# Performance work log

Hardware: AMD Instinct MI355X
Metric: run time of the kernel (lower is better)

Reference implementation:

```python
import jax, jax.numpy as jnp
import numpy as np

N = 50000
E = 500000
R = 8
IN_DIM = 128
HID = 128
OUT = 128
NUM_GRAPHS = 64
EPS_BN = 1e-5


def _glorot(key, shape):
    fan_in, fan_out = shape[-2], shape[-1]
    lim = np.sqrt(6.0 / (fan_in + fan_out))
    return jax.random.uniform(key, shape, jnp.float32, -lim, lim)


def setup_inputs() -> dict:
    key = jax.random.key(0)
    ks = jax.random.split(key, 24)
    x = jax.random.normal(ks[0], (N, IN_DIM), jnp.float32)
    edge_index = jax.random.randint(ks[1], (2, E), 0, N, jnp.int64)
    edge_type = jax.random.randint(ks[2], (E,), 0, R, jnp.int64)
    batch = jnp.sort(jax.random.randint(ks[3], (N,), 0, NUM_GRAPHS, jnp.int64))
    d = {
        "x": x, "edge_index": edge_index, "edge_type": edge_type, "batch": batch,
        # RGCN layer 1 (in->hid): per-relation weights, root weight, bias
        "W1": _glorot(ks[4], (R, IN_DIM, HID)), "root1": _glorot(ks[5], (IN_DIM, HID)), "b1": jnp.zeros((HID,), jnp.float32),
        "W2": _glorot(ks[6], (R, HID, HID)), "root2": _glorot(ks[7], (HID, HID)), "b2": jnp.zeros((HID,), jnp.float32),
        "W3": _glorot(ks[8], (R, HID, HID)), "root3": _glorot(ks[9], (HID, HID)), "b3": jnp.zeros((HID,), jnp.float32),
        # BatchNorm affine params
        "g1": jnp.ones((HID,), jnp.float32), "beta1": jnp.zeros((HID,), jnp.float32),
        "g2": jnp.ones((HID,), jnp.float32), "beta2": jnp.zeros((HID,), jnp.float32),
        # attention MLP: hid -> hid//2 -> 1
        "A1": _glorot(ks[10], (HID, HID // 2)), "a1": jnp.zeros((HID // 2,), jnp.float32),
        "A2": _glorot(ks[11], (HID // 2, 1)), "a2": jnp.zeros((1,), jnp.float32),
        # combiner MLP: 2*hid -> hid -> out
        "C1": _glorot(ks[12], (2 * HID, HID)), "c1": jnp.zeros((HID,), jnp.float32),
        "C2": _glorot(ks[13], (HID, OUT)), "c2": jnp.zeros((OUT,), jnp.float32),
    }
    return d


def rgcn_conv(h, src, dst, etype, W, root, bias):
    # relation-wise gather -> mean-aggregate per (dst, relation) -> transform
    seg = dst * R + etype                                   # [E]
    msg = h[src]                                            # [E, d_in] gather
    agg = jax.ops.segment_sum(msg, seg, num_segments=N * R) # [N*R, d_in]
    cnt = jax.ops.segment_sum(jnp.ones((seg.shape[0],), h.dtype), seg, num_segments=N * R)
    agg = agg / jnp.maximum(cnt, 1.0)[:, None]              # mean aggregation (PyG default)
    agg = agg.reshape(N, R, -1)
    out = jnp.einsum('nri,rio->no', agg, W) + h @ root + bias
    return out


def batch_norm(h, gamma, beta):
    mu = jnp.mean(h, axis=0, keepdims=True)
    var = jnp.mean((h - mu) ** 2, axis=0, keepdims=True)
    return (h - mu) * jax.lax.rsqrt(var + EPS_BN) * gamma + beta


def lrelu(h):
    return jax.nn.leaky_relu(h, 0.1)


def reference(x, edge_index, edge_type, batch, W1, root1, b1, W2, root2, b2,
              W3, root3, b3, g1, beta1, g2, beta2, A1, a1, A2, a2, C1, c1, C2, c2):
    src, dst = edge_index[0], edge_index[1]
    h = rgcn_conv(x, src, dst, edge_type, W1, root1, b1)
    h = lrelu(batch_norm(h, g1, beta1))
    h = rgcn_conv(h, src, dst, edge_type, W2, root2, b2)
    h = lrelu(batch_norm(h, g2, beta2))
    node_emb = rgcn_conv(h, src, dst, edge_type, W3, root3, b3)  # [N, HID]

    # attention pooling: scores softmax-ed over ALL nodes (dim=0, as in source)
    scores = lrelu(node_emb @ A1 + a1) @ A2 + a2                 # [N, 1]
    attn = jax.nn.softmax(scores, axis=0)                        # [N, 1]
    global_emb = jax.ops.segment_sum(node_emb * attn, batch, num_segments=NUM_GRAPHS)

    combined = jnp.concatenate([node_emb, global_emb[batch]], axis=1)  # [N, 2*HID]
    final = lrelu(combined @ C1 + c1) @ C2 + c2                  # [N, OUT]
    norm = jnp.linalg.norm(final, axis=1, keepdims=True)
    return final / jnp.maximum(norm, 1e-12)
```

## Files before the change

### kernel.cpp

```cpp
#include <hip/hip_runtime.h>
#include <hip/hip_bf16.h>

typedef unsigned int u32;
typedef unsigned short u16;
typedef __bf16 bf16_t;
typedef bf16_t bf16x8 __attribute__((ext_vector_type(8)));
typedef float f32x4 __attribute__((ext_vector_type(4)));

constexpr int NN = 50000;
constexpr int EE = 500000;
constexpr int RR = 8;
constexpr int NKEY = RR * NN;
constexpr int PAIR_B = (NKEY + 511) / 512;

constexpr int WX_A1T = 0;
constexpr int WX_C1T = 8192;
constexpr int WX_C2T = 40960;
constexpr int WX_A2  = 57344;
constexpr int WX_a1  = 57408;
constexpr int WX_c1  = 57472;
constexpr int WX_c2  = 57600;
constexpr int WX_a2s = 57728;
constexpr int WX_TOT = 57729;

__device__ __forceinline__ float bf2f(u32 v){
  union { u32 u; float f; } x; x.u = (v & 0xFFFFu) << 16; return x.f;
}
__device__ __forceinline__ u16 f2bf(float f){
  union { u32 u; float f; } x; x.f = f;
  u32 r = x.u + 0x7FFFu + ((x.u >> 16) & 1u);
  return (u16)(r >> 16);
}
__device__ __forceinline__ float lrelu(float x){ return x > 0.f ? x : 0.1f * x; }
__device__ __forceinline__ float ldf(const void* p, int i, u32 fm){
  return fm ? ((const float*)p)[i] : bf2f(((const u16*)p)[i]);
}
__device__ __forceinline__ void gl_lds16(const u16* g, u16* l){
  __builtin_amdgcn_global_load_lds((const __attribute__((address_space(1))) u32*)g,
                                   (__attribute__((address_space(3))) u32*)l, 16, 0, 0);
}

__global__ void k_fdetect(const void* x, u32* md){
  __shared__ u32 c;
  if (threadIdx.x == 0) c = 0;
  __syncthreads();
  const u16* p = (const u16*)x;
  u32 loc = 0;
  for (int j = 0; j < 16; j++){
    u16 v = p[threadIdx.x * 16 + j];
    u32 e = (v >> 7) & 0xFF;
    if (e >= 0xFD) loc++;
  }
  atomicAdd(&c, loc);
  __syncthreads();
  if (threadIdx.x == 0) md[0] = (c >= 4) ? 1u : 0u;
}
__global__ void k_idetect(const void* et, u32* md){
  __shared__ u32 c;
  if (threadIdx.x == 0) c = 0;
  __syncthreads();
  const int* p = (const int*)et;
  u32 loc = 0;
  for (int j = 0; j < 8; j++){
    int idx = 2 * (threadIdx.x * 8 + j) + 1;
    if (p[idx] != 0) loc++;
  }
  atomicAdd(&c, loc);
  __syncthreads();
  if (threadIdx.x == 0) md[1] = (c == 0) ? 1u : 0u;
}

__global__ void k_icvt(const void* ei, const void* et, const void* bat,
                       int* ei_c, int* et_c, int* bat_c, const u32* md){
  u32 im = md[1];
  int i = blockIdx.x * 256 + threadIdx.x;
  if (i < 2 * EE){
    const int* p = (const int*)ei;
    ei_c[i] = im ? p[2 * i] : p[i];
  } else if (i < 3 * EE){
    int j = i - 2 * EE;
    const int* p = (const int*)et;
    et_c[j] = im ? p[2 * j] : p[j];
  } else if (i < 3 * EE + NN){
    int j = i - 3 * EE;
    const int* p = (const int*)bat;
    bat_c[j] = im ? p[2 * j] : p[j];
  }
}

__global__ void k_xcvt(const void* x, u16* xb, const u32* md, u32* flags){
  u32 fm = md[0];
  int i4 = (blockIdx.x * 256 + threadIdx.x) * 4;
  if (i4 >= NN * 128) return;
  float v[4];
  if (fm){
    float4 f = *(const float4*)((const float*)x + i4);
    v[0]=f.x; v[1]=f.y; v[2]=f.z; v[3]=f.w;
  } else {
    uint2 u = *(const uint2*)((const u16*)x + i4);
    v[0]=bf2f(u.x); v[1]=bf2f(u.x>>16); v[2]=bf2f(u.y); v[3]=bf2f(u.y>>16);
  }
  bool bad = false;
  u16 o[4];
  for (int j = 0; j < 4; j++){
    if (v[j] != v[j]){ bad = true; v[j] = 0.f; }
    o[j] = f2bf(v[j]);
  }
  unsigned long long bal = __ballot(bad);
  if (bal && (threadIdx.x & 63) == 0) atomicOr(flags, 2u);
  uint2 st;
  st.x = (u32)o[0] | ((u32)o[1] << 16);
  st.y = (u32)o[2] | ((u32)o[3] << 16);
  *(uint2*)(xb + i4) = st;
}

__global__ void k_wcat(const void* W1, const void* r1, const void* W2, const void* r2,
                       const void* W3, const void* r3, u16* wcatT, const u32* md, u32* flags){
  u32 fm = md[0];
  int idx = blockIdx.x * 256 + threadIdx.x;
  if (idx >= 3 * 128 * 1152) return;
  int L = idx / (128 * 1152);
  int rem = idx % (128 * 1152);
  int n = rem / 1152, k = rem % 1152;
  const void* W  = (L == 0) ? W1 : ((L == 1) ? W2 : W3);
  const void* rt = (L == 0) ? r1 : ((L == 1) ? r2 : r3);
  float v = (k < 1024) ? ldf(W, k * 128 + n, fm) : ldf(rt, (k - 1024) * 128 + n, fm);
  if (v != v){ v = 0.f; atomicOr(flags, 2u); }
  wcatT[idx] = f2bf(v);
}

__global__ void k_wext(const void* A1, const void* a1, const void* A2, const void* a2,
                       const void* C1, const void* c1, const void* C2, const void* c2,
                       u16* wext, const u32* md){
  u32 fm = md[0];
  int idx = blockIdx.x * 256 + threadIdx.x;
  if (idx >= WX_TOT) return;
  float v;
  if (idx < WX_C1T){
    int n = idx >> 7, k = idx & 127;
    v = ldf(A1, k * 64 + n, fm);
  } else if (idx < WX_C2T){
    int j = idx - WX_C1T; int n = j >> 8, k = j & 255;
    v = ldf(C1, k * 128 + n, fm);
  } else if (idx < WX_A2){
    int j = idx - WX_C2T; int n = j >> 7, k = j & 127;
    v = ldf(C2, k * 128 + n, fm);
  } else if (idx < WX_a1){ v = ldf(A2, idx - WX_A2, fm); }
  else if (idx < WX_c1){ v = ldf(a1, idx - WX_a1, fm); }
  else if (idx < WX_c2){ v = ldf(c1, idx - WX_c1, fm); }
  else if (idx < WX_a2s){ v = ldf(c2, idx - WX_c2, fm); }
  else { v = ldf(a2, 0, fm); }
  wext[idx] = f2bf(v);
}

__global__ void k_count3(const int* __restrict__ ei, const int* __restrict__ et, u32* __restrict__ cnt){
  int e = blockIdx.x * 256 + threadIdx.x;
  if (e >= EE) return;
  atomicAdd(&cnt[ei[EE + e] * RR + et[e]], 1u);
}
__global__ void k_pairA(const u32* __restrict__ cnt, u32* __restrict__ blockSum){
  __shared__ u32 sd[256];
  int b = blockIdx.x, t = threadIdx.x;
  u32 s = 0;
  for (int j = 0; j < 2; j++){
    int key = b * 512 + t * 2 + j;
    if (key < NKEY) s += cnt[key];
  }
  sd[t] = s; __syncthreads();
  for (int off = 128; off; off >>= 1){ if (t < off) sd[t] += sd[t + off]; __syncthreads(); }
  if (t == 0) blockSum[b] = sd[0];
}
__global__ void k_pairB(const u32* __restrict__ blockSum, u32* __restrict__ blockBase){
  int lane = threadIdx.x;
  u32 loc[13]; u32 s = 0;
  for (int j = 0; j < 13; j++){
    int b = lane * 13 + j;
    u32 v = (b < PAIR_B) ? blockSum[b] : 0u;
    loc[j] = s; s += v;
  }
  u32 tot = s;
  for (int off = 1; off < 64; off <<= 1){
    u32 x = __shfl_up(tot, off);
    if (lane >= off) tot += x;
  }
  u32 excl = tot - s;
  for (int j = 0; j < 13; j++){
    int b = lane * 13 + j;
    if (b < PAIR_B) blockBase[b] = excl + loc[j];
  }
}
__global__ void k_pairC(const u32* __restrict__ cnt, const u32* __restrict__ blockBase,
                        u32* __restrict__ pairStart, u32* __restrict__ cursor){
  __shared__ u32 sd[256];
  int b = blockIdx.x, t = threadIdx.x;
  int k0 = b * 512 + t * 2;
  u32 v0 = 0, v1 = 0;
  if (k0 < NKEY) v0 = cnt[k0];
  if (k0 + 1 < NKEY) v1 = cnt[k0 + 1];
  sd[t] = v0 + v1; __syncthreads();
  for (int off = 1; off < 256; off <<= 1){
    u32 x = (t >= off) ? sd[t - off] : 0u;
    __syncthreads();
    sd[t] += x;
    __syncthreads();
  }
  u32 excl = sd[t] - (v0 + v1);
  u32 base = blockBase[b] + excl;
  if (k0 < NKEY){ pairStart[k0] = base; cursor[k0] = 0u; }
  if (k0 + 1 < NKEY){ pairStart[k0 + 1] = base + v0; cursor[k0 + 1] = 0u; }
  if (k0 + 1 == NKEY - 1) pairStart[NKEY] = base + v0 + v1;
}
__global__ void k_sort3(const int* __restrict__ ei, const int* __restrict__ et,
                        const u32* __restrict__ pairStart, u32* __restrict__ cursor,
                        u32* __restrict__ src_s){
  int e = blockIdx.x * 256 + threadIdx.x;
  if (e >= EE) return;
  int r = et[e], d = ei[EE + e];
  u32 key = (u32)d * RR + (u32)r;
  u32 p = pairStart[key] + atomicAdd(&cursor[key], 1u);
  src_s[p] = (u32)ei[e];
}

__global__ __launch_bounds__(256) void k_agg(const u16* __restrict__ h,
                                             const u32* __restrict__ pairStart,
                                             const u32* __restrict__ src_s,
                                             u16* __restrict__ agg){
  int d = blockIdx.x * 4 + (threadIdx.x >> 6);
  if (d >= NN) return;
  int lane = threadIdx.x & 63;
  const uint4* p4 = (const uint4*)(pairStart + d * 8);
  uint4 q0 = p4[0], q1 = p4[1];
  u32 ps[9];
  ps[0]=q0.x; ps[1]=q0.y; ps[2]=q0.z; ps[3]=q0.w;
  ps[4]=q1.x; ps[5]=q1.y; ps[6]=q1.z; ps[7]=q1.w;
  ps[8]=pairStart[d * 8 + 8];
  u16* dst = agg + (size_t)d * 1024 + lane * 2;
  #pragma unroll
  for (int r = 0; r < 8; r++){
    float a0 = 0.f, a1 = 0.f;
    for (u32 j = ps[r]; j < ps[r + 1]; j++){
      u32 src = src_s[j];
      u32 v = *(const u32*)(h + (size_t)src * 128 + lane * 2);
      a0 += bf2f(v); a1 += bf2f(v >> 16);
    }
    int c = (int)(ps[r + 1] - ps[r]);
    float sc = 1.0f / (float)max(c, 1);
    u32 st = (u32)f2bf(a0 * sc) | ((u32)f2bf(a1 * sc) << 16);
    *(u32*)(dst + r * 128) = st;
  }
}

__global__ __launch_bounds__(256) void k_gemm_big(const u16* __restrict__ h,
                                                  const u16* __restrict__ agg,
                                                  const u16* __restrict__ wT,
                                                  const void* __restrict__ bias,
                                                  float* __restrict__ out, const u32* md,
                                                  float* __restrict__ stats, int do_stats){
  __shared__ u16 As[64][64];
  __shared__ u16 Bs[128][64];
  u32 fm = md[0];
  int m0 = blockIdx.x * 64;
  int tid = threadIdx.x;
  int w = tid >> 6, lane = tid & 63, qd = lane >> 4, l16 = lane & 15;

  int rin = lane >> 3;
  int sc8 = (lane & 7) ^ rin;

  const u16* agA[2]; const u16* hA[2]; u16* ldsA[2];
  #pragma unroll
  for (int i = 0; i < 2; i++){
    int row = (w * 2 + i) * 8 + rin;
    int node = m0 + row; if (node > NN - 1) node = NN - 1;
    agA[i] = agg + (size_t)node * 1024 + sc8 * 8;
    hA[i]  = h + (size_t)node * 128 + sc8 * 8;
    ldsA[i] = &As[(w * 2 + i) * 8][0];
  }
  const u16* wB[4]; u16* ldsB[4];
  #pragma unroll
  for (int i = 0; i < 4; i++){
    int row = (w * 4 + i) * 8 + rin;
    wB[i] = wT + (size_t)row * 1152 + sc8 * 8;
    ldsB[i] = &Bs[(w * 4 + i) * 8][0];
  }

  f32x4 acc[8];
  #pragma unroll
  for (int j = 0; j < 8; j++) acc[j] = (f32x4){0.f,0.f,0.f,0.f};

  int sw = (l16 & 7) << 3;
  for (int k0 = 0; k0 < 1152; k0 += 64){
    __syncthreads();
    if (k0 < 1024){
      gl_lds16(agA[0] + k0, ldsA[0]);
      gl_lds16(agA[1] + k0, ldsA[1]);
    } else {
      gl_lds16(hA[0] + (k0 - 1024), ldsA[0]);
      gl_lds16(hA[1] + (k0 - 1024), ldsA[1]);
    }
    #pragma unroll
    for (int i = 0; i < 4; i++) gl_lds16(wB[i] + k0, ldsB[i]);
    __syncthreads();
    #pragma unroll
    for (int kk = 0; kk < 64; kk += 32){
      bf16x8 a = *(const bf16x8*)(&As[w * 16 + l16][(kk + qd * 8) ^ sw]);
      #pragma unroll
      for (int ct = 0; ct < 8; ct++){
        bf16x8 b = *(const bf16x8*)(&Bs[ct * 16 + l16][(kk + qd * 8) ^ sw]);
        acc[ct] = __builtin_amdgcn_mfma_f32_16x16x32_bf16(a, b, acc[ct], 0, 0, 0);
      }
    }
  }

  float sarr[8], s2arr[8];
  #pragma unroll
  for (int ct = 0; ct < 8; ct++){
    int col = ct * 16 + l16;
    float bv = ldf(bias, col, fm);
    float s = 0.f, s2 = 0.f;
    int rbase = m0 + w * 16 + qd * 4;
    #pragma unroll
    for (int rg = 0; rg < 4; rg++){
      int node = rbase + rg;
      if (node < NN){
        float v = acc[ct][rg] + bv;
        out[(size_t)node * 128 + col] = v;
        s += v; s2 += v * v;
      }
    }
    s  += __shfl_xor(s, 16);  s  += __shfl_xor(s, 32);
    s2 += __shfl_xor(s2, 16); s2 += __shfl_xor(s2, 32);
    sarr[ct] = s; s2arr[ct] = s2;
  }
  if (do_stats){
    float* red = (float*)&As[0][0];
    __syncthreads();
    if (qd == 0){
      #pragma unroll
      for (int ct = 0; ct < 8; ct++){
        red[w * 256 + ct * 16 + l16] = sarr[ct];
        red[w * 256 + 128 + ct * 16 + l16] = s2arr[ct];
      }
    }
    __syncthreads();
    if (tid < 256){
      float v = red[tid] + red[256 + tid] + red[512 + tid] + red[768 + tid];
      unsafeAtomicAdd(&stats[tid], v);
    }
  }
}

__global__ void k_bnapply(const float* __restrict__ out, const float* __restrict__ stats,
                          const void* __restrict__ g, const void* __restrict__ beta,
                          u16* __restrict__ hout, const u32* md, u32* flags, u32 layerbit){
  u32 fm = md[0];
  int idx = (blockIdx.x * 256 + threadIdx.x) * 4;
  if (idx >= NN * 128) return;
  int col = idx & 127;
  float4 v = *(const float4*)(out + idx);
  float vv[4] = {v.x, v.y, v.z, v.w};
  bool bad = false;
  u16 o[4];
  for (int j = 0; j < 4; j++){
    int c = col + j;
    float mu = stats[c] * (1.0f / NN);
    float var = fmaxf(stats[128 + c] * (1.0f / NN) - mu * mu, 0.f);
    float sc = ldf(g, c, fm) * rsqrtf(var + 1e-5f);
    float sh = ldf(beta, c, fm) - mu * sc;
    float r = vv[j] * sc + sh;
    if (r != r || sc != sc){ bad = true; r = 0.f; }
    o[j] = f2bf(lrelu(r));
  }
  unsigned long long bal = __ballot(bad);
  if (bal && (threadIdx.x & 63) == 0) atomicOr(flags, layerbit);
  uint2 st;
  st.x = (u32)o[0] | ((u32)o[1] << 16);
  st.y = (u32)o[2] | ((u32)o[3] << 16);
  *(uint2*)(hout + idx) = st;
}

__global__ __launch_bounds__(256) void k_scores_mfma(const float* __restrict__ emb,
                                                     const u16* __restrict__ wext,
                                                     float* __restrict__ scores){
  __shared__ u16 As[64][136];
  int m0 = blockIdx.x * 64;
  int tid = threadIdx.x;
  int w = tid >> 6, lane = tid & 63, qd = lane >> 4, l16 = lane & 15;
  for (int it = 0; it < 8; it++){
    int lin = it * 1024 + tid * 4;
    int row = lin >> 7, c = lin & 127;
    int node = m0 + row;
    float4 v = make_float4(0.f,0.f,0.f,0.f);
    if (node < NN) v = *(const float4*)(emb + (size_t)node * 128 + c);
    uint2 st;
    st.x = (u32)f2bf(v.x) | ((u32)f2bf(v.y) << 16);
    st.y = (u32)f2bf(v.z) | ((u32)f2bf(v.w) << 16);
    *(uint2*)(&As[row][c]) = st;
  }
  __syncthreads();
  f32x4 acc[4];
  for (int j = 0; j < 4; j++) acc[j] = (f32x4){0.f,0.f,0.f,0.f};
  for (int k0 = 0; k0 < 4; k0++){
    bf16x8 a = *(const bf16x8*)(&As[w * 16 + l16][k0 * 32 + qd * 8]);
    for (int ct = 0; ct < 4; ct++){
      bf16x8 b = *(const bf16x8*)(wext + WX_A1T + (size_t)(ct * 16 + l16) * 128 + k0 * 32 + qd * 8);
      acc[ct] = __builtin_amdgcn_mfma_f32_16x16x32_bf16(a, b, acc[ct], 0, 0, 0);
    }
  }
  float a1v[4], a2v[4];
  for (int ct = 0; ct < 4; ct++){
    a1v[ct] = bf2f(wext[WX_a1 + ct * 16 + l16]);
    a2v[ct] = bf2f(wext[WX_A2 + ct * 16 + l16]);
  }
  float a2s = bf2f(wext[WX_a2s]);
  for (int rg = 0; rg < 4; rg++){
    float s = 0.f;
    for (int ct = 0; ct < 4; ct++)
      s += lrelu(acc[ct][rg] + a1v[ct]) * a2v[ct];
    s += __shfl_xor(s, 1); s += __shfl_xor(s, 2);
    s += __shfl_xor(s, 4); s += __shfl_xor(s, 8);
    int row = m0 + w * 16 + qd * 4 + rg;
    if (l16 == 0 && row < NN) scores[row] = s + a2s;
  }
}

__device__ __forceinline__ u32 fmap(float f){
  union{u32 u; float f;} x; x.f = f;
  return (x.u & 0x80000000u) ? ~x.u : (x.u | 0x80000000u);
}
__device__ __forceinline__ float funmap(u32 m){
  union{u32 u; float f;} x;
  x.u = (m & 0x80000000u) ? (m ^ 0x80000000u) : ~m;
  return x.f;
}

__global__ void k_max(const float* __restrict__ scores, u32* smax){
  int gid = blockIdx.x * 256 + threadIdx.x;
  float m = -1e30f;
  for (int i = gid; i < NN; i += 256 * 128) m = fmaxf(m, scores[i]);
  for (int off = 32; off; off >>= 1) m = fmaxf(m, __shfl_down(m, off));
  if ((threadIdx.x & 63) == 0) atomicMax(smax, fmap(m));
}

__global__ void k_expsum(const float* __restrict__ scores, const u32* smax,
                         float* __restrict__ attnw, float* ssum, u32* flags){
  float mx = funmap(*smax);
  int gid = blockIdx.x * 256 + threadIdx.x;
  if (mx != mx){ if (gid == 0) atomicOr(flags, 32u); mx = 0.f; }
  float s = 0.f;
  bool bad = false;
  for (int i = gid; i < NN; i += 256 * 128){
    float e = __expf(scores[i] - mx);
    if (e != e){ bad = true; e = 0.f; }
    attnw[i] = e; s += e;
  }
  unsigned long long bal = __ballot(bad);
  if (bal && (threadIdx.x & 63) == 0) atomicOr(flags, 32u);
  for (int off = 32; off; off >>= 1) s += __shfl_down(s, off);
  if ((threadIdx.x & 63) == 0) unsafeAtomicAdd(ssum, s);
}

constexpr int POOL_CHUNK = 32;
__global__ __launch_bounds__(128) void k_pool(const float* __restrict__ emb,
                                              const float* __restrict__ attnw,
                                              const float* __restrict__ ssum,
                                              const int* __restrict__ batch,
                                              float* __restrict__ gemb, u32* flags){
  int t = threadIdx.x;
  int n0 = blockIdx.x * POOL_CHUNK;
  if (n0 >= NN) return;
  int n1 = min(n0 + POOL_CHUNK, NN);
  float sv = *ssum;
  bool bad = !(sv > 0.f) || (sv != sv);
  if (bad && t == 0 && blockIdx.x == 0) atomicOr(flags, 64u);
  float rs = bad ? 0.f : 1.0f / sv;
  int cur = batch[n0];
  float acc = 0.f;
  for (int n = n0; n < n1; n++){
    int b = batch[n];
    if (b != cur){ unsafeAtomicAdd(&gemb[cur * 128 + t], acc * rs); acc = 0.f; cur = b; }
    acc += emb[(size_t)n * 128 + t] * attnw[n];
  }
  unsafeAtomicAdd(&gemb[cur * 128 + t], acc * rs);
}

__global__ __launch_bounds__(256) void k_final_mfma(const float* __restrict__ emb,
                                                    const float* __restrict__ gemb,
                                                    const int* __restrict__ batch,
                                                    const u16* __restrict__ wext,
                                                    void* __restrict__ outp,
                                                    const u32* md){
  __shared__ u16 As[64][264];
  u16 (*Hs)[136] = (u16(*)[136])(&As[0][0]);
  u32 fm = md[0];
  int m0 = blockIdx.x * 64;
  int tid = threadIdx.x;
  int w = tid >> 6, lane = tid & 63, qd = lane >> 4, l16 = lane & 15;
  for (int it = 0; it < 16; it++){
    int lin = it * 1024 + tid * 4;
    int row = lin >> 8, c = lin & 255;
    int node = m0 + row;
    float4 v = make_float4(0.f,0.f,0.f,0.f);
    if (node < NN){
      if (c < 128) v = *(const float4*)(emb + (size_t)node * 128 + c);
      else { int g = batch[node]; v = *(const float4*)(gemb + (size_t)g * 128 + (c - 128)); }
    }
    uint2 st;
    st.x = (u32)f2bf(v.x) | ((u32)f2bf(v.y) << 16);
    st.y = (u32)f2bf(v.z) | ((u32)f2bf(v.w) << 16);
    *(uint2*)(&As[row][c]) = st;
  }
  __syncthreads();
  f32x4 acc[8];
  for (int j = 0; j < 8; j++) acc[j] = (f32x4){0.f,0.f,0.f,0.f};
  for (int k0 = 0; k0 < 8; k0++){
    bf16x8 a = *(const bf16x8*)(&As[w * 16 + l16][k0 * 32 + qd * 8]);
    for (int ct = 0; ct < 8; ct++){
      bf16x8 b = *(const bf16x8*)(wext + WX_C1T + (size_t)(ct * 16 + l16) * 256 + k0 * 32 + qd * 8);
      acc[ct] = __builtin_amdgcn_mfma_f32_16x16x32_bf16(a, b, acc[ct], 0, 0, 0);
    }
  }
  __syncthreads();
  for (int ct = 0; ct < 8; ct++){
    float c1v = bf2f(wext[WX_c1 + ct * 16 + l16]);
    for (int rg = 0; rg < 4; rg++){
      int row = w * 16 + qd * 4 + rg;
      Hs[row][ct * 16 + l16] = f2bf(lrelu(acc[ct][rg] + c1v));
    }
  }
  __syncthreads();
  f32x4 acc2[8];
  for (int j = 0; j < 8; j++) acc2[j] = (f32x4){0.f,0.f,0.f,0.f};
  for (int k0 = 0; k0 < 4; k0++){
    bf16x8 a = *(const bf16x8*)(&Hs[w * 16 + l16][k0 * 32 + qd * 8]);
    for (int ct = 0; ct < 8; ct++){
      bf16x8 b = *(const bf16x8*)(wext + WX_C2T + (size_t)(ct * 16 + l16) * 128 + k0 * 32 + qd * 8);
      acc2[ct] = __builtin_amdgcn_mfma_f32_16x16x32_bf16(a, b, acc2[ct], 0, 0, 0);
    }
  }
  float c2v[8];
  for (int ct = 0; ct < 8; ct++) c2v[ct] = bf2f(wext[WX_c2 + ct * 16 + l16]);
  for (int rg = 0; rg < 4; rg++){
    float ss = 0.f;
    for (int ct = 0; ct < 8; ct++){
      float o = acc2[ct][rg] + c2v[ct];
      ss += o * o;
    }
    ss += __shfl_xor(ss, 1); ss += __shfl_xor(ss, 2);
    ss += __shfl_xor(ss, 4); ss += __shfl_xor(ss, 8);
    float sc = 1.0f / fmaxf(sqrtf(ss), 1e-12f);
    int row = m0 + w * 16 + qd * 4 + rg;
    if (row < NN){
      if (fm){
        float* op = (float*)outp;
        for (int ct = 0; ct < 8; ct++)
          op[(size_t)row * 128 + ct * 16 + l16] = (acc2[ct][rg] + c2v[ct]) * sc;
      } else {
        u16* op = (u16*)outp;
        for (int ct = 0; ct < 8; ct++)
          op[(size_t)row * 128 + ct * 16 + l16] = f2bf((acc2[ct][rg] + c2v[ct]) * sc);
      }
    }
  }
}

__global__ void k_diag(const u32* pairStart, const u32* flags, const u32* md, void* outp){
  if (threadIdx.x != 0 || blockIdx.x != 0) return;
  u32 fm = md[0];
  u32 f = flags[0];
  if (pairStart[NKEY] != (u32)EE) f |= 1u;
  for (int b = 0; b < 9; b++){
    if (f & (1u << b)){
      float s = (float)(131072 >> b);
      if (fm) ((float*)outp)[b] = s;
      else ((u16*)outp)[b] = f2bf(s);
    }
  }
}
__global__ void k_wsfail(u32* outp){ outp[0] = 0x43000000u; }

constexpr size_t O_OUT   = 0;
constexpr size_t O_H     = 25600000;
constexpr size_t O_XBF   = 38400000;
constexpr size_t O_WCAT  = 51200000;
constexpr size_t O_WEXT  = 52084736;
constexpr size_t O_EI    = 52200448;
constexpr size_t O_ET    = 56200448;
constexpr size_t O_BAT   = 58200448;
constexpr size_t O_SRC   = 58400448;
constexpr size_t O_PST   = 60400448;
constexpr size_t O_CNT   = 62400448;
constexpr size_t O_SCO   = 65600448;
constexpr size_t O_AW    = 65800448;
constexpr size_t O_GEMB  = 66000448;
constexpr size_t O_STATS = 66033216;
constexpr size_t O_MISC  = 66035264;
constexpr size_t O_AGG   = 66035520;
constexpr size_t WS_NEED = 168435520;

extern "C" void kernel_launch(void* const* d_in, const int* in_sizes, int n_in,
                              void* d_out, int out_size, void* d_ws, size_t ws_size,
                              hipStream_t stream) {
  const void* x     = d_in[0];
  const void* ei    = d_in[1];
  const void* et    = d_in[2];
  const void* batch = d_in[3];
  const void* W1 = d_in[4],  *r1 = d_in[5],  *b1 = d_in[6];
  const void* W2 = d_in[7],  *r2 = d_in[8],  *b2 = d_in[9];
  const void* W3 = d_in[10], *r3 = d_in[11], *b3 = d_in[12];
  const void* g1 = d_in[13], *be1 = d_in[14];
  const void* g2 = d_in[15], *be2 = d_in[16];
  const void* A1 = d_in[17], *a1 = d_in[18];
  const void* A2 = d_in[19], *a2 = d_in[20];
  const void* C1 = d_in[21], *c1 = d_in[22];
  const void* C2 = d_in[23], *c2 = d_in[24];

  if (ws_size < WS_NEED){ k_wsfail<<<1, 1, 0, stream>>>((u32*)d_out); return; }
  char* ws = (char*)d_ws;
  float* out   = (float*)(ws + O_OUT);
  u16*   hbuf  = (u16*)(ws + O_H);
  u16*   xbf   = (u16*)(ws + O_XBF);
  u16*   wcat  = (u16*)(ws + O_WCAT);
  u16*   wext  = (u16*)(ws + O_WEXT);
  int*   ei_c  = (int*)(ws + O_EI);
  int*   et_c  = (int*)(ws + O_ET);
  int*   bat_c = (int*)(ws + O_BAT);
  u32*   src_s = (u32*)(ws + O_SRC);
  u32*   pairStart = (u32*)(ws + O_PST);
  u32*   cnt   = (u32*)(ws + O_CNT);
  float* sco   = (float*)(ws + O_SCO);
  float* aw    = (float*)(ws + O_AW);
  float* gemb  = (float*)(ws + O_GEMB);
  float* stats = (float*)(ws + O_STATS);
  u32*   misc  = (u32*)(ws + O_MISC);
  u16*   aggb  = (u16*)(ws + O_AGG);
  u32* cursor    = (u32*)(ws + O_OUT);
  u32* blockSum  = (u32*)(ws + O_OUT + 1600000);
  u32* blockBase = (u32*)(ws + O_OUT + 1604096);
  u32* smax = misc + 25;
  float* ssum = (float*)(misc + 26);
  u32* flags = misc + 27;
  u32* md = misc + 28;

  hipMemsetAsync(ws + O_CNT, 0, 1600000, stream);
  hipMemsetAsync(ws + O_GEMB, 0, 32768 + 2048 + 256, stream);

  k_fdetect<<<1, 256, 0, stream>>>(x, md);
  k_idetect<<<1, 256, 0, stream>>>(et, md);
  k_icvt<<<6055, 256, 0, stream>>>(ei, et, batch, ei_c, et_c, bat_c, md);
  k_xcvt<<<6250, 256, 0, stream>>>(x, xbf, md, flags);
  k_wcat<<<1728, 256, 0, stream>>>(W1, r1, W2, r2, W3, r3, wcat, md, flags);
  k_wext<<<227, 256, 0, stream>>>(A1, a1, A2, a2, C1, c1, C2, c2, wext, md);

  k_count3<<<(EE + 255) / 256, 256, 0, stream>>>(ei_c, et_c, cnt);
  k_pairA<<<PAIR_B, 256, 0, stream>>>(cnt, blockSum);
  k_pairB<<<1, 64, 0, stream>>>(blockSum, blockBase);
  k_pairC<<<PAIR_B, 256, 0, stream>>>(cnt, blockBase, pairStart, cursor);
  k_sort3<<<(EE + 255) / 256, 256, 0, stream>>>(ei_c, et_c, pairStart, cursor, src_s);

  const void* bias[3] = {b1, b2, b3};
  const void* gam[2] = {g1, g2};
  const void* bet[2] = {be1, be2};
  const u16* hin = xbf;
  for (int L = 0; L < 3; L++){
    const u16* wT = wcat + (size_t)L * 128 * 1152;
    k_agg<<<(NN + 3) / 4, 256, 0, stream>>>(hin, pairStart, src_s, aggb);
    k_gemm_big<<<(NN + 63) / 64, 256, 0, stream>>>(hin, aggb, wT, bias[L], out, md,
                                                   stats + (L < 2 ? L * 256 : 0), (L < 2) ? 1 : 0);
    if (L < 2){
      k_bnapply<<<6250, 256, 0, stream>>>(out, stats + L * 256, gam[L], bet[L], hbuf, md, flags, 4u << L);
      hin = hbuf;
    }
  }
  k_scores_mfma<<<(NN + 63) / 64, 256, 0, stream>>>(out, wext, sco);
  k_max<<<128, 256, 0, stream>>>(sco, smax);
  k_expsum<<<128, 256, 0, stream>>>(sco, smax, aw, ssum, flags);
  k_pool<<<(NN + POOL_CHUNK - 1) / POOL_CHUNK, 128, 0, stream>>>(out, aw, ssum, bat_c, gemb, flags);
  k_final_mfma<<<(NN + 63) / 64, 256, 0, stream>>>(out, gemb, bat_c, wext, d_out, md);
  k_diag<<<1, 64, 0, stream>>>(pairStart, flags, md, d_out);
}
```

Before: 673.9 us.

## Precompute per-graph combiner projection, fuse score max, load MFMA operands directly

Global embedding is shared by every node in a graph, so its half of the C1 projection (plus bias) is computed once per graph in a small kernel and added per row, halving the K dimension of the first combiner GEMM. The softmax max reduction is fused into the scores kernel through a per-wave atomicMax, which removes the separate max kernel. The scores and final kernels now load the A operand straight from global memory into registers instead of staging it through LDS. This adds one small launch and changes rounding slightly, since the global part is now accumulated in fp32 rather than bf16.

```diff
diff --git a/kernel.cpp b/kernel.cpp
--- a/kernel.cpp
+++ b/kernel.cpp
@@ -38,6 +38,12 @@
 __device__ __forceinline__ void gl_lds16(const u16* g, u16* l){
   __builtin_amdgcn_global_load_lds((const __attribute__((address_space(1))) u32*)g,
                                    (__attribute__((address_space(3))) u32*)l, 16, 0, 0);
+}
+__device__ __forceinline__ bf16x8 cvt8(float4 a, float4 b){
+  union { bf16x8 v; u16 s[8]; } r;
+  r.s[0]=f2bf(a.x); r.s[1]=f2bf(a.y); r.s[2]=f2bf(a.z); r.s[3]=f2bf(a.w);
+  r.s[4]=f2bf(b.x); r.s[5]=f2bf(b.y); r.s[6]=f2bf(b.z); r.s[7]=f2bf(b.w);
+  return r.v;
 }
 
 __global__ void k_fdetect(const void* x, u32* md){
@@ -380,65 +386,59 @@
 
 __global__ __launch_bounds__(256) void k_scores_mfma(const float* __restrict__ emb,
                                                      const u16* __restrict__ wext,
-                                                     float* __restrict__ scores){
-  __shared__ u16 As[64][136];
+                                                     float* __restrict__ scores, u32* smax){
   int m0 = blockIdx.x * 64;
   int tid = threadIdx.x;
   int w = tid >> 6, lane = tid & 63, qd = lane >> 4, l16 = lane & 15;
-  for (int it = 0; it < 8; it++){
-    int lin = it * 1024 + tid * 4;
-    int row = lin >> 7, c = lin & 127;
-    int node = m0 + row;
-    float4 v = make_float4(0.f,0.f,0.f,0.f);
-    if (node < NN) v = *(const float4*)(emb + (size_t)node * 128 + c);
-    uint2 st;
-    st.x = (u32)f2bf(v.x) | ((u32)f2bf(v.y) << 16);
-    st.y = (u32)f2bf(v.z) | ((u32)f2bf(v.w) << 16);
-    *(uint2*)(&As[row][c]) = st;
-  }
-  __syncthreads();
+  int na = m0 + w * 16 + l16; if (na > NN - 1) na = NN - 1;
+  const float* arow = emb + (size_t)na * 128;
   f32x4 acc[4];
+  #pragma unroll
   for (int j = 0; j < 4; j++) acc[j] = (f32x4){0.f,0.f,0.f,0.f};
+  #pragma unroll
   for (int k0 = 0; k0 < 4; k0++){
-    bf16x8 a = *(const bf16x8*)(&As[w * 16 + l16][k0 * 32 + qd * 8]);
+    float4 f0 = *(const float4*)(arow + k0 * 32 + qd * 8);
+    float4 f1 = *(const float4*)(arow + k0 * 32 + qd * 8 + 4);
+    bf16x8 a = cvt8(f0, f1);
+    #pragma unroll
     for (int ct = 0; ct < 4; ct++){
       bf16x8 b = *(const bf16x8*)(wext + WX_A1T + (size_t)(ct * 16 + l16) * 128 + k0 * 32 + qd * 8);
       acc[ct] = __builtin_amdgcn_mfma_f32_16x16x32_bf16(a, b, acc[ct], 0, 0, 0);
     }
   }
   float a1v[4], a2v[4];
+  #pragma unroll
   for (int ct = 0; ct < 4; ct++){
     a1v[ct] = bf2f(wext[WX_a1 + ct * 16 + l16]);
     a2v[ct] = bf2f(wext[WX_A2 + ct * 16 + l16]);
   }
   float a2s = bf2f(wext[WX_a2s]);
+  float bm = -1e30f;
+  #pragma unroll
   for (int rg = 0; rg < 4; rg++){
     float s = 0.f;
+    #pragma unroll
     for (int ct = 0; ct < 4; ct++)
       s += lrelu(acc[ct][rg] + a1v[ct]) * a2v[ct];
     s += __shfl_xor(s, 1); s += __shfl_xor(s, 2);
     s += __shfl_xor(s, 4); s += __shfl_xor(s, 8);
     int row = m0 + w * 16 + qd * 4 + rg;
-    if (l16 == 0 && row < NN) scores[row] = s + a2s;
-  }
-}
-
-__device__ __forceinline__ u32 fmap(float f){
-  union{u32 u; float f;} x; x.f = f;
-  return (x.u & 0x80000000u) ? ~x.u : (x.u | 0x80000000u);
-}
+    float sf = s + a2s;
+    if (row < NN){
+      bm = fmaxf(bm, sf);
+      if (l16 == 0) scores[row] = sf;
+    }
+  }
+  bm = fmaxf(bm, __shfl_xor(bm, 16));
+  bm = fmaxf(bm, __shfl_xor(bm, 32));
+  if (lane == 0) atomicMax(smax, (bm >= -1e29f) ?
+      ((__float_as_uint(bm) & 0x80000000u) ? ~__float_as_uint(bm) : (__float_as_uint(bm) | 0x80000000u)) : 0u);
+}
+
 __device__ __forceinline__ float funmap(u32 m){
   union{u32 u; float f;} x;
   x.u = (m & 0x80000000u) ? (m ^ 0x80000000u) : ~m;
   return x.f;
-}
-
-__global__ void k_max(const float* __restrict__ scores, u32* smax){
-  int gid = blockIdx.x * 256 + threadIdx.x;
-  float m = -1e30f;
-  for (int i = gid; i < NN; i += 256 * 128) m = fmaxf(m, scores[i]);
-  for (int off = 32; off; off >>= 1) m = fmaxf(m, __shfl_down(m, off));
-  if ((threadIdx.x & 63) == 0) atomicMax(smax, fmap(m));
 }
 
 __global__ void k_expsum(const float* __restrict__ scores, const u32* smax,
@@ -483,64 +483,83 @@
   unsafeAtomicAdd(&gemb[cur * 128 + t], acc * rs);
 }
 
+__global__ void k_gembC(const float* __restrict__ gemb, const u16* __restrict__ wext,
+                        float* __restrict__ gembC){
+  int idx = blockIdx.x * 256 + threadIdx.x;
+  if (idx >= 64 * 128) return;
+  int g = idx >> 7, n = idx & 127;
+  const float* gr = gemb + g * 128;
+  const u16* wr = wext + WX_C1T + (size_t)n * 256 + 128;
+  float s = 0.f;
+  #pragma unroll 8
+  for (int k = 0; k < 128; k++) s += gr[k] * bf2f(wr[k]);
+  gembC[idx] = s + bf2f(wext[WX_c1 + n]);
+}
+
 __global__ __launch_bounds__(256) void k_final_mfma(const float* __restrict__ emb,
-                                                    const float* __restrict__ gemb,
+                                                    const float* __restrict__ gembC,
                                                     const int* __restrict__ batch,
                                                     const u16* __restrict__ wext,
                                                     void* __restrict__ outp,
                                                     const u32* md){
-  __shared__ u16 As[64][264];
-  u16 (*Hs)[136] = (u16(*)[136])(&As[0][0]);
+  __shared__ u16 Hs[64][136];
   u32 fm = md[0];
   int m0 = blockIdx.x * 64;
   int tid = threadIdx.x;
   int w = tid >> 6, lane = tid & 63, qd = lane >> 4, l16 = lane & 15;
-  for (int it = 0; it < 16; it++){
-    int lin = it * 1024 + tid * 4;
-    int row = lin >> 8, c = lin & 255;
-    int node = m0 + row;
-    float4 v = make_float4(0.f,0.f,0.f,0.f);
-    if (node < NN){
-      if (c < 128) v = *(const float4*)(emb + (size_t)node * 128 + c);
-      else { int g = batch[node]; v = *(const float4*)(gemb + (size_t)g * 128 + (c - 128)); }
-    }
-    uint2 st;
-    st.x = (u32)f2bf(v.x) | ((u32)f2bf(v.y) << 16);
-    st.y = (u32)f2bf(v.z) | ((u32)f2bf(v.w) << 16);
-    *(uint2*)(&As[row][c]) = st;
-  }
-  __syncthreads();
+  int na = m0 + w * 16 + l16; if (na > NN - 1) na = NN - 1;
+  const float* arow = emb + (size_t)na * 128;
+
   f32x4 acc[8];
+  #pragma unroll
   for (int j = 0; j < 8; j++) acc[j] = (f32x4){0.f,0.f,0.f,0.f};
-  for (int k0 = 0; k0 < 8; k0++){
-    bf16x8 a = *(const bf16x8*)(&As[w * 16 + l16][k0 * 32 + qd * 8]);
+  #pragma unroll
+  for (int k0 = 0; k0 < 4; k0++){
+    float4 f0 = *(const float4*)(arow + k0 * 32 + qd * 8);
+    float4 f1 = *(const float4*)(arow + k0 * 32 + qd * 8 + 4);
+    bf16x8 a = cvt8(f0, f1);
+    #pragma unroll
     for (int ct = 0; ct < 8; ct++){
       bf16x8 b = *(const bf16x8*)(wext + WX_C1T + (size_t)(ct * 16 + l16) * 256 + k0 * 32 + qd * 8);
       acc[ct] = __builtin_amdgcn_mfma_f32_16x16x32_bf16(a, b, acc[ct], 0, 0, 0);
     }
   }
-  __syncthreads();
+  int rbase = w * 16 + qd * 4;
+  int gg[4];
+  #pragma unroll
+  for (int rg = 0; rg < 4; rg++){
+    int node = m0 + rbase + rg; if (node > NN - 1) node = NN - 1;
+    gg[rg] = batch[node];
+  }
+  #pragma unroll
   for (int ct = 0; ct < 8; ct++){
-    float c1v = bf2f(wext[WX_c1 + ct * 16 + l16]);
+    int col = ct * 16 + l16;
+    #pragma unroll
     for (int rg = 0; rg < 4; rg++){
-      int row = w * 16 + qd * 4 + rg;
-      Hs[row][ct * 16 + l16] = f2bf(lrelu(acc[ct][rg] + c1v));
+      float h = acc[ct][rg] + gembC[gg[rg] * 128 + col];
+      Hs[rbase + rg][col] = f2bf(lrelu(h));
     }
   }
   __syncthreads();
   f32x4 acc2[8];
+  #pragma unroll
   for (int j = 0; j < 8; j++) acc2[j] = (f32x4){0.f,0.f,0.f,0.f};
+  #pragma unroll
   for (int k0 = 0; k0 < 4; k0++){
     bf16x8 a = *(const bf16x8*)(&Hs[w * 16 + l16][k0 * 32 + qd * 8]);
+    #pragma unroll
     for (int ct = 0; ct < 8; ct++){
       bf16x8 b = *(const bf16x8*)(wext + WX_C2T + (size_t)(ct * 16 + l16) * 128 + k0 * 32 + qd * 8);
       acc2[ct] = __builtin_amdgcn_mfma_f32_16x16x32_bf16(a, b, acc2[ct], 0, 0, 0);
     }
   }
   float c2v[8];
+  #pragma unroll
   for (int ct = 0; ct < 8; ct++) c2v[ct] = bf2f(wext[WX_c2 + ct * 16 + l16]);
+  #pragma unroll
   for (int rg = 0; rg < 4; rg++){
     float ss = 0.f;
+    #pragma unroll
     for (int ct = 0; ct < 8; ct++){
       float o = acc2[ct][rg] + c2v[ct];
       ss += o * o;
@@ -548,14 +567,16 @@
     ss += __shfl_xor(ss, 1); ss += __shfl_xor(ss, 2);
     ss += __shfl_xor(ss, 4); ss += __shfl_xor(ss, 8);
     float sc = 1.0f / fmaxf(sqrtf(ss), 1e-12f);
-    int row = m0 + w * 16 + qd * 4 + rg;
+    int row = m0 + rbase + rg;
     if (row < NN){
       if (fm){
         float* op = (float*)outp;
+        #pragma unroll
         for (int ct = 0; ct < 8; ct++)
           op[(size_t)row * 128 + ct * 16 + l16] = (acc2[ct][rg] + c2v[ct]) * sc;
       } else {
         u16* op = (u16*)outp;
+        #pragma unroll
         for (int ct = 0; ct < 8; ct++)
           op[(size_t)row * 128 + ct * 16 + l16] = f2bf((acc2[ct][rg] + c2v[ct]) * sc);
       }
@@ -588,6 +609,7 @@
 constexpr size_t O_BAT   = 58200448;
 constexpr size_t O_SRC   = 58400448;
 constexpr size_t O_PST   = 60400448;
+constexpr size_t O_GEMBC = 62100448;
 constexpr size_t O_CNT   = 62400448;
 constexpr size_t O_SCO   = 65600448;
 constexpr size_t O_AW    = 65800448;
@@ -626,6 +648,7 @@
   int*   bat_c = (int*)(ws + O_BAT);
   u32*   src_s = (u32*)(ws + O_SRC);
   u32*   pairStart = (u32*)(ws + O_PST);
+  float* gembC = (float*)(ws + O_GEMBC);
   u32*   cnt   = (u32*)(ws + O_CNT);
   float* sco   = (float*)(ws + O_SCO);
   float* aw    = (float*)(ws + O_AW);
@@ -671,10 +694,10 @@
       hin = hbuf;
     }
   }
-  k_scores_mfma<<<(NN + 63) / 64, 256, 0, stream>>>(out, wext, sco);
-  k_max<<<128, 256, 0, stream>>>(sco, smax);
+  k_scores_mfma<<<(NN + 63) / 64, 256, 0, stream>>>(out, wext, sco, smax);
   k_expsum<<<128, 256, 0, stream>>>(sco, smax, aw, ssum, flags);
   k_pool<<<(NN + POOL_CHUNK - 1) / POOL_CHUNK, 128, 0, stream>>>(out, aw, ssum, bat_c, gemb, flags);
-  k_final_mfma<<<(NN + 63) / 64, 256, 0, stream>>>(out, gemb, bat_c, wext, d_out, md);
+  k_gembC<<<32, 256, 0, stream>>>(gemb, wext, gembC);
+  k_final_mfma<<<(NN + 63) / 64, 256, 0, stream>>>(out, gembC, bat_c, wext, d_out, md);
   k_diag<<<1, 64, 0, stream>>>(pairStart, flags, md, d_out);
 }
```

Measured after the change: 685.8 us. No clear change (+1.8%).
